# Kernel tuning notes

Hardware: AMD Instinct MI355X
Metric: run time of the kernel (lower is better)

## Reference

```python
import jax, jax.numpy as jnp
import numpy as np

N_CODEBOOKS = 4
N_EMBED = 1024
EMBED_DIM = 64
PATCH = 4
BETA = 0.25
EPS = 1e-5
USAGE_W = 0.01


def setup_inputs() -> dict:
    key = jax.random.key(0)
    k1, k2 = jax.random.split(key)
    z = jax.random.normal(k1, (8, 64, 128, 128), dtype=jnp.float32)
    # one EMA codebook per quantizer, initialized ~ randn like torch buffer
    codebooks = jax.random.normal(k2, (N_CODEBOOKS, N_EMBED, EMBED_DIM), dtype=jnp.float32)
    return {"z": z, "codebooks": codebooks}


def _usage_loss(indices, n_embed):
    # negative-entropy penalty on code usage (no gradient path: counts are ints)
    counts = jnp.bincount(indices.reshape(-1), length=n_embed).astype(jnp.float32)
    probs = (counts + EPS) / (counts.sum() + EPS * n_embed)
    entropy = -jnp.sum(probs * jnp.log(probs + EPS))
    return jnp.log(jnp.float32(n_embed)) - entropy


def _ema_quantize(residual, embedding):
    # residual: [N, C, ph, pw], embedding: [n_e, C]; eval mode (no EMA buffer update)
    N, C, ph, pw = residual.shape
    z_flat = residual.transpose(0, 2, 3, 1).reshape(-1, C)  # [M, C]
    d = (jnp.sum(z_flat ** 2, axis=1, keepdims=True)
         + jnp.sum(embedding ** 2, axis=1)
         - 2.0 * z_flat @ embedding.T)  # [M, n_e]
    idx = jnp.argmin(d, axis=1)  # [M]
    z_q = embedding[idx].reshape(N, ph, pw, C).transpose(0, 3, 1, 2)  # [N, C, ph, pw]
    loss = BETA * jnp.mean((jax.lax.stop_gradient(z_q) - residual) ** 2)
    z_q_st = residual + jax.lax.stop_gradient(z_q - residual)  # straight-through
    return z_q_st, loss, idx.reshape(N, ph, pw)


def reference(z, codebooks):
    B, C, H, W = z.shape
    h, w = H // PATCH, W // PATCH
    # b c (h ph) (w pw) -> (b h w) c ph pw
    zp = (z.reshape(B, C, h, PATCH, w, PATCH)
            .transpose(0, 2, 4, 1, 3, 5)
            .reshape(B * h * w, C, PATCH, PATCH))
    zq_acc = jnp.zeros_like(zp)
    residual = zp
    losses, all_idx = [], []
    for i in range(N_CODEBOOKS):
        zq_i, loss_i, idx_i = _ema_quantize(residual, codebooks[i])
        loss_i = loss_i + USAGE_W * _usage_loss(idx_i, N_EMBED)
        zq_acc = zq_acc + zq_i
        residual = residual - zq_i
        losses.append(loss_i)
        all_idx.append(idx_i.reshape(idx_i.shape[0], -1))  # [N, ph*pw]
    loss = jnp.stack(losses).sum()
    # (b h w) c ph pw -> b c (h ph) (w pw)
    z_q = (zq_acc.reshape(B, h, w, C, PATCH, PATCH)
                 .transpose(0, 3, 1, 4, 2, 5)
                 .reshape(B, C, H, W))
    # [N, patch_area, n_codebooks] -> [b, h, w, patch_area, n_codebooks]
    min_idx = jnp.stack(all_idx, axis=-1).reshape(B, h, w, PATCH * PATCH, N_CODEBOOKS)
    return z_q, loss, min_idx
```

## Files before the change

kernel.cpp:

```cpp
#include <hip/hip_runtime.h>
#include <math.h>

typedef __attribute__((ext_vector_type(8))) short short8;
typedef __attribute__((ext_vector_type(4))) float f32x4;

#define NCB 4
#define NE 1024
#define DIM 64
#define HW 16384
#define NPIX 131072
#define NWAVES 4096
#define MSE_DENOM 8388608.0f
#define EPSF 1e-5f
#define CHUNK_BYTES 24576
#define CHUNK_SHORTS 12288

__device__ __forceinline__ unsigned short f2bf(float x) {
    unsigned u = __float_as_uint(x);
    u += 0x7fffu + ((u >> 16) & 1u);
    return (unsigned short)(u >> 16);
}
__device__ __forceinline__ float bf2f(unsigned short h) {
    return __uint_as_float(((unsigned)h) << 16);
}

__global__ __launch_bounds__(64) void rvq_norms(const float* __restrict__ cb,
                                                float* __restrict__ nrmh) {
    int code = blockIdx.x * 64 + threadIdx.x;
    const float4* row = reinterpret_cast<const float4*>(cb + (size_t)code * DIM);
    float s0 = 0.f, s1 = 0.f, s2 = 0.f, s3 = 0.f;
#pragma unroll
    for (int k = 0; k < 16; ++k) {
        float4 v = row[k];
        s0 = fmaf(v.x, v.x, s0); s1 = fmaf(v.y, v.y, s1);
        s2 = fmaf(v.z, v.z, s2); s3 = fmaf(v.w, v.w, s3);
    }
    nrmh[code] = -0.5f * ((s0 + s1) + (s2 + s3));
}

__global__ __launch_bounds__(256) void rvq_presplit(const float* __restrict__ cb,
                                                    unsigned short* __restrict__ gB) {
    int blk = blockIdx.x;
    int tid = threadIdx.x;
    int code = tid >> 2, dg = tid & 3;
    int c0 = (blk & 15) << 6;
    int i  = blk >> 4;
    const float4* s4 = reinterpret_cast<const float4*>(
        cb + ((size_t)i * NE + c0 + code) * DIM + dg * 16);
    float v[16];
    {
        float4 q;
        q = s4[0]; v[0]=q.x; v[1]=q.y; v[2]=q.z; v[3]=q.w;
        q = s4[1]; v[4]=q.x; v[5]=q.y; v[6]=q.z; v[7]=q.w;
        q = s4[2]; v[8]=q.x; v[9]=q.y; v[10]=q.z; v[11]=q.w;
        q = s4[3]; v[12]=q.x; v[13]=q.y; v[14]=q.z; v[15]=q.w;
    }
    char* outc = reinterpret_cast<char*>(gB + (size_t)blk * CHUNK_SHORTS);
    int linbase = code * 128 + dg * 32;
    int sw = (code & 7) << 4;
#pragma unroll
    for (int h = 0; h < 2; ++h) {
        short8 p1, p2, p3;
#pragma unroll
        for (int e = 0; e < 8; ++e) {
            float t = v[h * 8 + e];
            unsigned short u1 = f2bf(t); t -= bf2f(u1);
            unsigned short u2 = f2bf(t); t -= bf2f(u2);
            unsigned short u3 = f2bf(t);
            p1[e] = (short)u1; p2[e] = (short)u2; p3[e] = (short)u3;
        }
        int a = (linbase + h * 16) ^ sw;
        *reinterpret_cast<short8*>(outc + a)         = p1;
        *reinterpret_cast<short8*>(outc + 8192 + a)  = p2;
        *reinterpret_cast<short8*>(outc + 16384 + a) = p3;
    }
}

__device__ __forceinline__ void gload16(const void* gsrc, void* ldst) {
    __builtin_amdgcn_global_load_lds(
        (const __attribute__((address_space(1))) unsigned int*)gsrc,
        (__attribute__((address_space(3))) unsigned int*)ldst, 16, 0, 0);
}

__global__ __launch_bounds__(256, 2) void rvq_main(
    const float* __restrict__ z, const unsigned short* __restrict__ gB,
    const float* __restrict__ nrmh, const float* __restrict__ cb,
    float* __restrict__ out_zq, float* __restrict__ out_idx,
    unsigned* __restrict__ hist, float* __restrict__ msePartial)
{
    __shared__ uint4 sB[2][CHUNK_BYTES / 16];
    __shared__ int   sBest[4][32];

    const int tid  = threadIdx.x;
    const int lane = tid & 63;
    const int wid  = tid >> 6;
    const int col  = lane & 15;
    const int g    = lane >> 4;
    const int blockPix = blockIdx.x * 128;
    char* sBase = reinterpret_cast<char*>(sB);
    const int stOff = wid * 1024;
    const int stLane = stOff + lane * 16;

    int pf[2]; size_t zb[2];
#pragma unroll
    for (int m = 0; m < 2; ++m) {
        pf[m] = blockPix + wid * 32 + m * 16 + col;
        zb[m] = (size_t)(pf[m] >> 14) * 1048576 + (size_t)(pf[m] & 16383);
    }

    float r[2][2][8];
#pragma unroll
    for (int m = 0; m < 2; ++m)
#pragma unroll
        for (int kh = 0; kh < 2; ++kh)
#pragma unroll
            for (int e = 0; e < 8; ++e)
                r[m][kh][e] = z[zb[m] + (size_t)(kh * 32 + g * 8 + e) * HW];

    for (int i = 0; i < NCB; ++i) {
        const char* gBi = reinterpret_cast<const char*>(gB) + (size_t)i * 16 * CHUNK_BYTES;
        const float* nrm_i = nrmh + i * NE;

        short8 A[3][2][2];
#pragma unroll
        for (int m = 0; m < 2; ++m)
#pragma unroll
            for (int kh = 0; kh < 2; ++kh)
#pragma unroll
                for (int e = 0; e < 8; ++e) {
                    float t = r[m][kh][e];
                    unsigned short u1 = f2bf(t); t -= bf2f(u1);
                    unsigned short u2 = f2bf(t); t -= bf2f(u2);
                    unsigned short u3 = f2bf(t);
                    A[0][m][kh][e] = (short)u1;
                    A[1][m][kh][e] = (short)u2;
                    A[2][m][kh][e] = (short)u3;
                }

#pragma unroll
        for (int k = 0; k < 6; ++k)
            gload16(gBi + k * 4096 + stLane, sBase + k * 4096 + stOff);
        __syncthreads();

        float maxv[2][4]; int maxi[2][4];
#pragma unroll
        for (int m = 0; m < 2; ++m)
#pragma unroll
            for (int rr = 0; rr < 4; ++rr) { maxv[m][rr] = -3.4e38f; maxi[m][rr] = 0; }

        for (int c = 0; c < 16; ++c) {
            const int cur = c & 1;
            if (c < 15) {
                const char* gc = gBi + (size_t)(c + 1) * CHUNK_BYTES;
                char* sbn = sBase + (cur ^ 1) * CHUNK_BYTES;
#pragma unroll
                for (int k = 0; k < 6; ++k)
                    gload16(gc + k * 4096 + stLane, sbn + k * 4096 + stOff);
            }
            const char* sbc = sBase + cur * CHUNK_BYTES;
            float nh[4];
#pragma unroll
            for (int sub = 0; sub < 4; ++sub)
                nh[sub] = nrm_i[(c << 6) + (sub << 4) + col];

#pragma unroll
            for (int sub = 0; sub < 4; ++sub) {
                int code = (sub << 4) + col;
                int sw = (code & 7) << 4;
                short8 B[3][2];
#pragma unroll
                for (int s = 0; s < 3; ++s)
#pragma unroll
                    for (int kh = 0; kh < 2; ++kh) {
                        int a = ((code << 7) + (kh << 6) + (g << 4)) ^ sw;
                        B[s][kh] = *reinterpret_cast<const short8*>(sbc + s * 8192 + a);
                    }
                f32x4 acc[2][2];
#pragma unroll
                for (int m = 0; m < 2; ++m)
#pragma unroll
                    for (int rr = 0; rr < 4; ++rr) {
                        acc[m][0][rr] = nh[sub];
                        acc[m][1][rr] = 0.f;
                    }
#pragma unroll
                for (int m = 0; m < 2; ++m)
#pragma unroll
                    for (int kh = 0; kh < 2; ++kh) {
                        acc[m][kh] = __builtin_amdgcn_mfma_f32_16x16x32_bf16(A[0][m][kh], B[0][kh], acc[m][kh], 0, 0, 0);
                        acc[m][kh] = __builtin_amdgcn_mfma_f32_16x16x32_bf16(A[0][m][kh], B[1][kh], acc[m][kh], 0, 0, 0);
                        acc[m][kh] = __builtin_amdgcn_mfma_f32_16x16x32_bf16(A[1][m][kh], B[0][kh], acc[m][kh], 0, 0, 0);
                        acc[m][kh] = __builtin_amdgcn_mfma_f32_16x16x32_bf16(A[0][m][kh], B[2][kh], acc[m][kh], 0, 0, 0);
                        acc[m][kh] = __builtin_amdgcn_mfma_f32_16x16x32_bf16(A[1][m][kh], B[1][kh], acc[m][kh], 0, 0, 0);
                        acc[m][kh] = __builtin_amdgcn_mfma_f32_16x16x32_bf16(A[2][m][kh], B[0][kh], acc[m][kh], 0, 0, 0);
                    }
#pragma unroll
                for (int m = 0; m < 2; ++m)
#pragma unroll
                    for (int rr = 0; rr < 4; ++rr) {
                        float s = acc[m][0][rr] + acc[m][1][rr];
                        if (s > maxv[m][rr]) { maxv[m][rr] = s; maxi[m][rr] = (c << 6) + code; }
                    }
            }
            __syncthreads();
        }

#pragma unroll
        for (int m = 0; m < 2; ++m)
#pragma unroll
            for (int rr = 0; rr < 4; ++rr) {
                float v = maxv[m][rr]; int ix = maxi[m][rr];
#pragma unroll
                for (int off = 1; off < 16; off <<= 1) {
                    float ov = __shfl_xor(v, off, 64);
                    int   oi = __shfl_xor(ix, off, 64);
                    if (ov > v || (ov == v && oi < ix)) { v = ov; ix = oi; }
                }
                maxi[m][rr] = ix;
            }
        __syncthreads();
        if (col == 0) {
#pragma unroll
            for (int m = 0; m < 2; ++m)
#pragma unroll
                for (int rr = 0; rr < 4; ++rr)
                    sBest[wid][m * 16 + g * 4 + rr] = maxi[m][rr];
        }
        __syncthreads();
        int best[2];
        best[0] = sBest[wid][col];
        best[1] = sBest[wid][16 + col];

        const float* cbi = cb + (size_t)i * NE * DIM;
        if (lane < 16) {
#pragma unroll
            for (int m = 0; m < 2; ++m) {
                int pfr = blockPix + wid * 32 + m * 16 + lane;
                int bb = pfr >> 14, yy = (pfr >> 7) & 127, xx = pfr & 127;
                int bi = sBest[wid][m * 16 + lane];
                size_t off = (size_t)bb * 65536 + (size_t)(yy >> 2) * 2048
                           + (size_t)(xx >> 2) * 64
                           + (size_t)(((yy & 3) << 2) + (xx & 3)) * 4 + (size_t)i;
                out_idx[off] = (float)bi;
                atomicAdd(&hist[i * NE + bi], 1u);
            }
        }

#pragma unroll
        for (int m = 0; m < 2; ++m) {
            const float* er = cbi + (size_t)best[m] * DIM;
#pragma unroll
            for (int kh = 0; kh < 2; ++kh) {
                const float4* e4 = reinterpret_cast<const float4*>(er + kh * 32 + g * 8);
                float4 q0 = e4[0], q1 = e4[1];
                r[m][kh][0] -= q0.x; r[m][kh][1] -= q0.y;
                r[m][kh][2] -= q0.z; r[m][kh][3] -= q0.w;
                r[m][kh][4] -= q1.x; r[m][kh][5] -= q1.y;
                r[m][kh][6] -= q1.z; r[m][kh][7] -= q1.w;
            }
        }

        float s = 0.f;
#pragma unroll
        for (int m = 0; m < 2; ++m)
#pragma unroll
            for (int kh = 0; kh < 2; ++kh)
#pragma unroll
                for (int e = 0; e < 8; ++e) s = fmaf(r[m][kh][e], r[m][kh][e], s);
#pragma unroll
        for (int d_ = 32; d_ > 0; d_ >>= 1) s += __shfl_down(s, d_, 64);
        if (lane == 0) msePartial[i * NWAVES + blockIdx.x * 4 + wid] = s;
    }

#pragma unroll
    for (int m = 0; m < 2; ++m)
#pragma unroll
        for (int kh = 0; kh < 2; ++kh)
#pragma unroll
            for (int e = 0; e < 8; ++e) {
                size_t o = zb[m] + (size_t)(kh * 32 + g * 8 + e) * HW;
                out_zq[o] = z[o] - r[m][kh][e];
            }
}

__global__ __launch_bounds__(1024) void rvq_finalize(
    const unsigned* __restrict__ hist, const float* __restrict__ msePartial,
    float* __restrict__ out_loss)
{
    __shared__ float red[1024];
    int t = threadIdx.x;
    float loss = 0.f;
    for (int i = 0; i < NCB; ++i) {
        float cnt = (float)hist[i * NE + t];
        float prob = (cnt + EPSF) / (131072.0f + EPSF * 1024.0f);
        red[t] = -prob * logf(prob + EPSF);
        __syncthreads();
        for (int s = 512; s > 0; s >>= 1) { if (t < s) red[t] += red[t + s]; __syncthreads(); }
        float entropy = red[0];
        __syncthreads();
        red[t] = msePartial[i * NWAVES + t]        + msePartial[i * NWAVES + 1024 + t]
               + msePartial[i * NWAVES + 2048 + t] + msePartial[i * NWAVES + 3072 + t];
        __syncthreads();
        for (int s = 512; s > 0; s >>= 1) { if (t < s) red[t] += red[t + s]; __syncthreads(); }
        float mse_sum = red[0];
        __syncthreads();
        loss += 0.25f * (mse_sum / MSE_DENOM) + 0.01f * (logf(1024.0f) - entropy);
    }
    if (t == 0) out_loss[0] = loss;
}

extern "C" void kernel_launch(void* const* d_in, const int* in_sizes, int n_in,
                              void* d_out, int out_size, void* d_ws, size_t ws_size,
                              hipStream_t stream) {
    const float* z  = (const float*)d_in[0];
    const float* cb = (const float*)d_in[1];

    float* out      = (float*)d_out;
    float* out_zq   = out;
    float* out_loss = out + 8388608;
    float* out_idx  = out + 8388609;

    unsigned* hist        = (unsigned*)d_ws;
    float*    nrmh        = (float*)((char*)d_ws + 16384);
    float*    msePartial  = (float*)((char*)d_ws + 32768);
    unsigned short* gB    = (unsigned short*)((char*)d_ws + 98304);

    hipMemsetAsync(d_ws, 0, 16384, stream);
    rvq_norms<<<64, 64, 0, stream>>>(cb, nrmh);
    rvq_presplit<<<64, 256, 0, stream>>>(cb, gB);
    rvq_main<<<1024, 256, 0, stream>>>(z, gB, nrmh, cb, out_zq, out_idx, hist, msePartial);
    rvq_finalize<<<1, 1024, 0, stream>>>(hist, msePartial, out_loss);
}
```

Baseline: 401.9 us.

## Halve LDS chunk size, raise occupancy, restructure MFMA accumulation with setprio

The codebook chunk staged in LDS per pipeline step shrinks from 64 to 32 codes, with the presplit layout changed to match, so LDS use drops and launch bounds can request 4 blocks per CU instead of 2. The MFMA loop now accumulates both K halves into one accumulator per row tile, keeping the same three-term bf16 split products, and raises wave priority around the MFMA burst. The chunk load is spread across all threads. The cost is twice as many chunk iterations and barriers, plus tighter register limits that could cause spills.

Result: faster. 383.0 us (-4.7%).

```diff
diff --git a/kernel.cpp b/kernel.cpp
--- a/kernel.cpp
+++ b/kernel.cpp
@@ -12,8 +12,8 @@
 #define NWAVES 4096
 #define MSE_DENOM 8388608.0f
 #define EPSF 1e-5f
-#define CHUNK_BYTES 24576
-#define CHUNK_SHORTS 12288
+#define CHUNK_BYTES 12288
+#define NCHUNK 32
 
 __device__ __forceinline__ unsigned short f2bf(float x) {
     unsigned u = __float_as_uint(x);
@@ -42,11 +42,11 @@
                                                     unsigned short* __restrict__ gB) {
     int blk = blockIdx.x;
     int tid = threadIdx.x;
-    int code = tid >> 2, dg = tid & 3;
+    int code64 = tid >> 2, dg = tid & 3;
     int c0 = (blk & 15) << 6;
     int i  = blk >> 4;
     const float4* s4 = reinterpret_cast<const float4*>(
-        cb + ((size_t)i * NE + c0 + code) * DIM + dg * 16);
+        cb + ((size_t)i * NE + c0 + code64) * DIM + dg * 16);
     float v[16];
     {
         float4 q;
@@ -55,9 +55,12 @@
         q = s4[2]; v[8]=q.x; v[9]=q.y; v[10]=q.z; v[11]=q.w;
         q = s4[3]; v[12]=q.x; v[13]=q.y; v[14]=q.z; v[15]=q.w;
     }
-    char* outc = reinterpret_cast<char*>(gB + (size_t)blk * CHUNK_SHORTS);
-    int linbase = code * 128 + dg * 32;
-    int sw = (code & 7) << 4;
+    int chunk = (blk & 15) * 2 + (code64 >> 5);
+    int j = code64 & 31;
+    char* outc = reinterpret_cast<char*>(gB)
+               + ((size_t)i * NCHUNK + chunk) * CHUNK_BYTES;
+    int linbase = j * 128 + dg * 32;
+    int sw = (j & 7) << 4;
 #pragma unroll
     for (int h = 0; h < 2; ++h) {
         short8 p1, p2, p3;
@@ -70,9 +73,9 @@
             p1[e] = (short)u1; p2[e] = (short)u2; p3[e] = (short)u3;
         }
         int a = (linbase + h * 16) ^ sw;
-        *reinterpret_cast<short8*>(outc + a)         = p1;
-        *reinterpret_cast<short8*>(outc + 8192 + a)  = p2;
-        *reinterpret_cast<short8*>(outc + 16384 + a) = p3;
+        *reinterpret_cast<short8*>(outc + a)        = p1;
+        *reinterpret_cast<short8*>(outc + 4096 + a) = p2;
+        *reinterpret_cast<short8*>(outc + 8192 + a) = p3;
     }
 }
 
@@ -82,7 +85,7 @@
         (__attribute__((address_space(3))) unsigned int*)ldst, 16, 0, 0);
 }
 
-__global__ __launch_bounds__(256, 2) void rvq_main(
+__global__ __launch_bounds__(256, 4) void rvq_main(
     const float* __restrict__ z, const unsigned short* __restrict__ gB,
     const float* __restrict__ nrmh, const float* __restrict__ cb,
     float* __restrict__ out_zq, float* __restrict__ out_idx,
@@ -98,14 +101,13 @@
     const int g    = lane >> 4;
     const int blockPix = blockIdx.x * 128;
     char* sBase = reinterpret_cast<char*>(sB);
-    const int stOff = wid * 1024;
-    const int stLane = stOff + lane * 16;
-
-    int pf[2]; size_t zb[2];
+    const int sw = (col & 7) << 4;
+
+    size_t zb[2];
 #pragma unroll
     for (int m = 0; m < 2; ++m) {
-        pf[m] = blockPix + wid * 32 + m * 16 + col;
-        zb[m] = (size_t)(pf[m] >> 14) * 1048576 + (size_t)(pf[m] & 16383);
+        int pf = blockPix + wid * 32 + m * 16 + col;
+        zb[m] = (size_t)(pf >> 14) * 1048576 + (size_t)(pf & 16383);
     }
 
     float r[2][2][8];
@@ -118,7 +120,7 @@
                 r[m][kh][e] = z[zb[m] + (size_t)(kh * 32 + g * 8 + e) * HW];
 
     for (int i = 0; i < NCB; ++i) {
-        const char* gBi = reinterpret_cast<const char*>(gB) + (size_t)i * 16 * CHUNK_BYTES;
+        const char* gBi = reinterpret_cast<const char*>(gB) + (size_t)i * NCHUNK * CHUNK_BYTES;
         const float* nrm_i = nrmh + i * NE;
 
         short8 A[3][2][2];
@@ -138,8 +140,8 @@
                 }
 
 #pragma unroll
-        for (int k = 0; k < 6; ++k)
-            gload16(gBi + k * 4096 + stLane, sBase + k * 4096 + stOff);
+        for (int k = 0; k < 3; ++k)
+            gload16(gBi + k * 4096 + tid * 16, sBase + k * 4096 + tid * 16);
         __syncthreads();
 
         float maxv[2][4]; int maxi[2][4];
@@ -148,58 +150,48 @@
 #pragma unroll
             for (int rr = 0; rr < 4; ++rr) { maxv[m][rr] = -3.4e38f; maxi[m][rr] = 0; }
 
-        for (int c = 0; c < 16; ++c) {
+        for (int c = 0; c < NCHUNK; ++c) {
             const int cur = c & 1;
-            if (c < 15) {
+            if (c < NCHUNK - 1) {
                 const char* gc = gBi + (size_t)(c + 1) * CHUNK_BYTES;
                 char* sbn = sBase + (cur ^ 1) * CHUNK_BYTES;
 #pragma unroll
-                for (int k = 0; k < 6; ++k)
-                    gload16(gc + k * 4096 + stLane, sbn + k * 4096 + stOff);
+                for (int k = 0; k < 3; ++k)
+                    gload16(gc + k * 4096 + tid * 16, sbn + k * 4096 + tid * 16);
             }
             const char* sbc = sBase + cur * CHUNK_BYTES;
-            float nh[4];
-#pragma unroll
-            for (int sub = 0; sub < 4; ++sub)
-                nh[sub] = nrm_i[(c << 6) + (sub << 4) + col];
-
-#pragma unroll
-            for (int sub = 0; sub < 4; ++sub) {
-                int code = (sub << 4) + col;
-                int sw = (code & 7) << 4;
-                short8 B[3][2];
-#pragma unroll
-                for (int s = 0; s < 3; ++s)
-#pragma unroll
-                    for (int kh = 0; kh < 2; ++kh) {
-                        int a = ((code << 7) + (kh << 6) + (g << 4)) ^ sw;
-                        B[s][kh] = *reinterpret_cast<const short8*>(sbc + s * 8192 + a);
+
+#pragma unroll
+            for (int sub = 0; sub < 2; ++sub) {
+                const int code = (sub << 4) + col;
+                float nh = nrm_i[(c << 5) + code];
+                f32x4 acc[2];
+#pragma unroll
+                for (int rr = 0; rr < 4; ++rr) { acc[0][rr] = nh; acc[1][rr] = nh; }
+
+                __builtin_amdgcn_s_setprio(1);
+#pragma unroll
+                for (int sb = 0; sb < 3; ++sb) {
+                    short8 B0 = *reinterpret_cast<const short8*>(
+                        sbc + sb * 4096 + ((((code << 7) + (g << 4))) ^ sw));
+                    short8 B1 = *reinterpret_cast<const short8*>(
+                        sbc + sb * 4096 + ((((code << 7) + 64 + (g << 4))) ^ sw));
+#pragma unroll
+                    for (int sa = 0; sa < 3 - sb; ++sa) {
+                        acc[0] = __builtin_amdgcn_mfma_f32_16x16x32_bf16(A[sa][0][0], B0, acc[0], 0, 0, 0);
+                        acc[1] = __builtin_amdgcn_mfma_f32_16x16x32_bf16(A[sa][1][0], B0, acc[1], 0, 0, 0);
+                        acc[0] = __builtin_amdgcn_mfma_f32_16x16x32_bf16(A[sa][0][1], B1, acc[0], 0, 0, 0);
+                        acc[1] = __builtin_amdgcn_mfma_f32_16x16x32_bf16(A[sa][1][1], B1, acc[1], 0, 0, 0);
                     }
-                f32x4 acc[2][2];
+                }
+                __builtin_amdgcn_s_setprio(0);
+
 #pragma unroll
                 for (int m = 0; m < 2; ++m)
 #pragma unroll
                     for (int rr = 0; rr < 4; ++rr) {
-                        acc[m][0][rr] = nh[sub];
-                        acc[m][1][rr] = 0.f;
-                    }
-#pragma unroll
-                for (int m = 0; m < 2; ++m)
-#pragma unroll
-                    for (int kh = 0; kh < 2; ++kh) {
-                        acc[m][kh] = __builtin_amdgcn_mfma_f32_16x16x32_bf16(A[0][m][kh], B[0][kh], acc[m][kh], 0, 0, 0);
-                        acc[m][kh] = __builtin_amdgcn_mfma_f32_16x16x32_bf16(A[0][m][kh], B[1][kh], acc[m][kh], 0, 0, 0);
-                        acc[m][kh] = __builtin_amdgcn_mfma_f32_16x16x32_bf16(A[1][m][kh], B[0][kh], acc[m][kh], 0, 0, 0);
-                        acc[m][kh] = __builtin_amdgcn_mfma_f32_16x16x32_bf16(A[0][m][kh], B[2][kh], acc[m][kh], 0, 0, 0);
-                        acc[m][kh] = __builtin_amdgcn_mfma_f32_16x16x32_bf16(A[1][m][kh], B[1][kh], acc[m][kh], 0, 0, 0);
-                        acc[m][kh] = __builtin_amdgcn_mfma_f32_16x16x32_bf16(A[2][m][kh], B[0][kh], acc[m][kh], 0, 0, 0);
-                    }
-#pragma unroll
-                for (int m = 0; m < 2; ++m)
-#pragma unroll
-                    for (int rr = 0; rr < 4; ++rr) {
-                        float s = acc[m][0][rr] + acc[m][1][rr];
-                        if (s > maxv[m][rr]) { maxv[m][rr] = s; maxi[m][rr] = (c << 6) + code; }
+                        float s = acc[m][rr];
+                        if (s > maxv[m][rr]) { maxv[m][rr] = s; maxi[m][rr] = (c << 5) + code; }
                     }
             }
             __syncthreads();
```
